# Optimization experiments

Measured on AMD Instinct MI355X. Metric: run time of the kernel, lower is better.

Reference implementation:

```python
import jax, jax.numpy as jnp
import numpy as np

CAPACITY_FACTOR = 1.25

def setup_inputs() -> dict:
    key = jax.random.key(0)
    ks = jax.random.split(key, 6)
    B, S, D, H, E = 4, 2048, 1024, 2048, 8
    x = jax.random.normal(ks[0], (B, S, D), dtype=jnp.float32)
    Wg = jax.random.normal(ks[1], (D, E), dtype=jnp.float32) / np.float32(np.sqrt(D))
    bg = jnp.zeros((E,), dtype=jnp.float32)
    W1 = jax.random.normal(ks[2], (E, H, D), dtype=jnp.float32) / np.float32(np.sqrt(H))
    W2 = jax.random.normal(ks[3], (E, D, H), dtype=jnp.float32) / np.float32(np.sqrt(D))
    W3 = jax.random.normal(ks[4], (E, D, H), dtype=jnp.float32) / np.float32(np.sqrt(D))
    return {"x": x, "Wg": Wg, "bg": bg, "W1": W1, "W2": W2, "W3": W3, "deterministic": 1}


def reference(x, Wg, bg, W1, W2, W3, deterministic):
    # deterministic=True path: no gate noise, no dropout (rate=0 anyway).
    b, s, d = x.shape
    E = W1.shape[0]
    xt = x.reshape(-1, d)                      # [N, d]
    N = xt.shape[0]
    cap = int(N / E * CAPACITY_FACTOR)

    logits = xt @ Wg + bg                      # [N, E]
    eid = jnp.argmax(logits, axis=1)           # [N] assigned expert (top-1)
    onehot = jax.nn.one_hot(eid, E, dtype=xt.dtype)
    # 0-based arrival position of each token within its expert's queue
    pos = (jnp.sum(jnp.cumsum(onehot, axis=0) * onehot, axis=1)).astype(jnp.int32) - 1
    valid = pos < cap                          # capacity mask (pos >= 0 always)
    slot = jnp.where(valid, pos, cap)          # overflow tokens -> dummy slot `cap`

    # Dispatch: scatter tokens into [E, cap+1, d]; slots unique among valid tokens
    buf = jnp.zeros((E, cap + 1, d), dtype=xt.dtype).at[eid, slot].set(xt)
    binp = buf[:, :cap]                        # [E, cap, d] (dummy slot dropped)

    # Grouped SwiGLU FFN per expert
    h = jax.nn.silu(jnp.einsum('ecd,edh->ech', binp, W2)) * jnp.einsum('ecd,edh->ech', binp, W3)
    bout = jnp.einsum('ech,ehd->ecd', h, W1)   # [E, cap, d]

    # Combine: gather each token's expert output; overflow tokens read zero row
    bout = jnp.concatenate([bout, jnp.zeros((E, 1, d), dtype=bout.dtype)], axis=1)
    eout = bout[eid, slot]                     # [N, d]

    weights = jax.nn.softmax(logits, axis=-1)
    gate_w = jnp.take_along_axis(weights, eid[:, None], axis=1)  # [N, 1]
    out = (gate_w * eout).reshape(b, s, d)
    return out
```

## Files before the change

### kernel.cpp

```cpp
#include <hip/hip_runtime.h>

#define N_TOK 8192
#define D_DIM 1024
#define H_DIM 2048
#define E_NUM 8
#define CAP   1280

typedef __attribute__((ext_vector_type(8))) short bf16x8;
typedef __attribute__((ext_vector_type(4))) float f32x4;

__device__ inline unsigned short f2bf(float f) {
  unsigned u = __float_as_uint(f);
  u += 0x7fffu + ((u >> 16) & 1u);
  return (unsigned short)(u >> 16);
}

#define VMCNT(n) asm volatile("s_waitcnt vmcnt(" #n ")" ::: "memory")
#define BARRIER() asm volatile("s_barrier" ::: "memory")

__global__ __launch_bounds__(256) void transpose_cvt_all(const float* __restrict__ W2,
                                                         const float* __restrict__ W3,
                                                         const float* __restrict__ W1,
                                                         unsigned short* __restrict__ w2t,
                                                         unsigned short* __restrict__ w3t,
                                                         unsigned short* __restrict__ w1t) {
  __shared__ float tile[64][33];
  const int id = blockIdx.x;
  const float* src;
  unsigned short* dst;
  int R, C, bx, by, b;
  if (id < 16384) {
    const int q = id & 8191;
    b = q >> 10;
    const int rem = q & 1023;
    bx = rem & 63;
    by = rem >> 6;
    R = D_DIM; C = H_DIM;
    src = (id < 8192 ? W2 : W3);
    dst = (id < 8192 ? w2t : w3t);
  } else {
    const int q = id - 16384;
    b = q >> 10;
    const int rem = q & 1023;
    bx = rem & 31;
    by = rem >> 5;
    R = H_DIM; C = D_DIM;
    src = W1; dst = w1t;
  }
  src += (size_t)b * R * C;
  dst += (size_t)b * R * C;
  const int c0 = bx * 32, r0 = by * 64;
  const int tx = threadIdx.x & 31, ty = threadIdx.x >> 5;
#pragma unroll
  for (int i = 0; i < 8; ++i)
    tile[ty + i * 8][tx] = src[(size_t)(r0 + ty + i * 8) * C + c0 + tx];
  __syncthreads();
  const int rp = threadIdx.x & 31;
  const int cb = threadIdx.x >> 5;
#pragma unroll
  for (int it = 0; it < 4; ++it) {
    const int c = cb + it * 8;
    unsigned short v[2] = {f2bf(tile[2 * rp][c]), f2bf(tile[2 * rp + 1][c])};
    *reinterpret_cast<unsigned*>(dst + (size_t)(c0 + c) * R + r0 + 2 * rp) =
        *reinterpret_cast<unsigned*>(v);
  }
}

__global__ __launch_bounds__(256) void gate_kernel(const float* __restrict__ x,
                                                   const float* __restrict__ Wg,
                                                   const float* __restrict__ bg,
                                                   int* __restrict__ eid,
                                                   float* __restrict__ gatew) {
  __shared__ float wg[E_NUM][D_DIM];
  const int tid = threadIdx.x;
  for (int i = tid; i < D_DIM * E_NUM; i += 256) {
    int d = i >> 3, e = i & 7;
    wg[e][d] = Wg[i];
  }
  __syncthreads();
  const int w = tid >> 6, l = tid & 63;
  const int t = blockIdx.x * 4 + w;
  const float* xr = x + (size_t)t * D_DIM;
  float acc[8] = {0, 0, 0, 0, 0, 0, 0, 0};
#pragma unroll
  for (int i = 0; i < D_DIM / 64; ++i) {
    float xv = xr[l + 64 * i];
#pragma unroll
    for (int e = 0; e < 8; ++e) acc[e] += xv * wg[e][l + 64 * i];
  }
#pragma unroll
  for (int off = 32; off >= 1; off >>= 1) {
#pragma unroll
    for (int e = 0; e < 8; ++e) acc[e] += __shfl_xor(acc[e], off);
  }
  if (l == 0) {
    float best = -1e30f;
    int bi = 0;
#pragma unroll
    for (int e = 0; e < 8; ++e) {
      acc[e] += bg[e];
      if (acc[e] > best) { best = acc[e]; bi = e; }
    }
    float s = 0.f;
#pragma unroll
    for (int e = 0; e < 8; ++e) s += __expf(acc[e] - best);
    eid[t] = bi;
    gatew[t] = 1.f / s;
  }
}

__global__ void scan_kernel(const int* __restrict__ eid, int* __restrict__ slot,
                            int* __restrict__ tok_of) {
  __shared__ int se[N_TOK];
  const int tid = threadIdx.x;
  for (int i = tid; i < N_TOK; i += 256) se[i] = eid[i];
  __syncthreads();
  if (tid >= 64) return;
  int counts[8] = {0, 0, 0, 0, 0, 0, 0, 0};
  const unsigned long long lower = (tid == 0) ? 0ull : ((1ull << tid) - 1ull);
  for (int base = 0; base < N_TOK; base += 64) {
    const int t = base + tid;
    const int e = se[t];
    int rank = 0;
#pragma unroll
    for (int ee = 0; ee < 8; ++ee) {
      unsigned long long m = __ballot(e == ee);
      if (e == ee) rank = counts[ee] + __popcll(m & lower);
      counts[ee] += __popcll(m);
    }
    slot[t] = rank < CAP ? rank : CAP;
    if (rank < CAP) tok_of[e * CAP + rank] = t;
  }
}

__global__ __launch_bounds__(256) void scatter_kernel(const float* __restrict__ x,
                                                      const int* __restrict__ tok_of,
                                                      unsigned short* __restrict__ binp) {
  const int row = blockIdx.x * 4 + (threadIdx.x >> 6);
  const int l = threadIdx.x & 63;
  const int t = tok_of[row];
  unsigned short* dst = binp + (size_t)row * D_DIM;
  if (t >= 0) {
    const float* src = x + (size_t)t * D_DIM;
#pragma unroll
    for (int i = 0; i < 4; ++i) {
      const int d = (i * 64 + l) * 4;
      float4 v = *reinterpret_cast<const float4*>(src + d);
      unsigned short r[4] = {f2bf(v.x), f2bf(v.y), f2bf(v.z), f2bf(v.w)};
      *reinterpret_cast<uint2*>(dst + d) = *reinterpret_cast<uint2*>(r);
    }
  } else {
    uint2 z = {0u, 0u};
#pragma unroll
    for (int i = 0; i < 4; ++i) {
      const int d = (i * 64 + l) * 4;
      *reinterpret_cast<uint2*>(dst + d) = z;
    }
  }
}

#define TILE64 (128 * 64)

__device__ inline void stage_tile(const unsigned short* __restrict__ g, int ldg, int k0,
                                  unsigned short* lds, int w, int l) {
  const int gcol = (l & 7) ^ (l >> 3);
  const unsigned short* gsrc = g + (size_t)(w * 32 + (l >> 3)) * ldg + k0 + gcol * 8;
#pragma unroll
  for (int it = 0; it < 4; ++it) {
    __builtin_amdgcn_global_load_lds(
        (const __attribute__((address_space(1))) unsigned int*)(gsrc + (size_t)(it * 8) * ldg),
        (__attribute__((address_space(3))) unsigned int*)(lds + (w * 32 + it * 8) * 64),
        16, 0, 0);
  }
}

__device__ inline bf16x8 lds_frag(const unsigned short* lds, int row, int c16) {
  return *reinterpret_cast<const bf16x8*>(lds + row * 64 + (c16 ^ (row & 7)) * 8);
}

__global__ __launch_bounds__(256, 2) void ffn1_kernel(const unsigned short* __restrict__ binp,
                                                      const unsigned short* __restrict__ w2t,
                                                      const unsigned short* __restrict__ w3t,
                                                      unsigned short* __restrict__ hbuf) {
  __shared__ unsigned short sA[2][TILE64], sB2[TILE64], sB3[TILE64];
  const int e = blockIdx.z, bx = blockIdx.x, by = blockIdx.y;
  const unsigned short* A  = binp + (size_t)e * CAP * D_DIM + (size_t)by * 128 * D_DIM;
  const unsigned short* B2 = w2t + (size_t)e * H_DIM * D_DIM + (size_t)bx * 128 * D_DIM;
  const unsigned short* B3 = w3t + (size_t)e * H_DIM * D_DIM + (size_t)bx * 128 * D_DIM;
  unsigned short* H = hbuf + (size_t)e * CAP * H_DIM;
  const int tid = threadIdx.x;
  const int l = tid & 63;
  const int w = tid >> 6, wr = w >> 1, wc = w & 1;
  f32x4 acc2[4][4] = {};
  f32x4 acc3[4][4] = {};

  stage_tile(A, D_DIM, 0, sA[0], w, l);

  const int NT = D_DIM / 64;
  int cur = 0;
  for (int kt = 0; kt < NT; ++kt) {
    stage_tile(B2, D_DIM, kt * 64, sB2, w, l);
    stage_tile(B3, D_DIM, kt * 64, sB3, w, l);
    if (kt + 1 < NT) {
      stage_tile(A, D_DIM, (kt + 1) * 64, sA[cur ^ 1], w, l);
      VMCNT(4);
    } else {
      VMCNT(0);
    }
    BARRIER();
#pragma unroll
    for (int kk = 0; kk < 2; ++kk) {
      const int c16 = kk * 4 + (l >> 4);
      bf16x8 af[4], b2f[4], b3f[4];
#pragma unroll
      for (int f = 0; f < 4; ++f) {
        af[f]  = lds_frag(sA[cur], wr * 64 + f * 16 + (l & 15), c16);
        b2f[f] = lds_frag(sB2, wc * 64 + f * 16 + (l & 15), c16);
        b3f[f] = lds_frag(sB3, wc * 64 + f * 16 + (l & 15), c16);
      }
#pragma unroll
      for (int fm = 0; fm < 4; ++fm)
#pragma unroll
        for (int fn = 0; fn < 4; ++fn) {
          acc2[fm][fn] = __builtin_amdgcn_mfma_f32_16x16x32_bf16(af[fm], b2f[fn], acc2[fm][fn], 0, 0, 0);
          acc3[fm][fn] = __builtin_amdgcn_mfma_f32_16x16x32_bf16(af[fm], b3f[fn], acc3[fm][fn], 0, 0, 0);
        }
    }
    BARRIER();
    cur ^= 1;
  }

  const int row0 = by * 128 + wr * 64;
  const int col0 = bx * 128 + wc * 64;
#pragma unroll
  for (int fm = 0; fm < 4; ++fm)
#pragma unroll
    for (int fn = 0; fn < 4; ++fn)
#pragma unroll
      for (int j = 0; j < 4; ++j) {
        const int row = row0 + fm * 16 + (l >> 4) * 4 + j;
        const int col = col0 + fn * 16 + (l & 15);
        const float v2 = acc2[fm][fn][j];
        const float v3 = acc3[fm][fn][j];
        const float hv = (v2 / (1.0f + __expf(-v2))) * v3;
        H[(size_t)row * H_DIM + col] = f2bf(hv);
      }
}

__global__ __launch_bounds__(256, 2) void ffn2_kernel(const unsigned short* __restrict__ hbuf,
                                                      const unsigned short* __restrict__ w1t,
                                                      const int* __restrict__ tok_of,
                                                      const float* __restrict__ gatew,
                                                      float* __restrict__ out) {
  __shared__ unsigned short sA[2][TILE64], sB[TILE64];
  const int e = blockIdx.z;
  const unsigned short* A = hbuf + (size_t)e * CAP * H_DIM + (size_t)blockIdx.y * 128 * H_DIM;
  const unsigned short* B = w1t + (size_t)e * D_DIM * H_DIM + (size_t)blockIdx.x * 128 * H_DIM;
  const int* tok = tok_of + e * CAP;
  const int tid = threadIdx.x;
  const int l = tid & 63;
  const int w = tid >> 6, wr = w >> 1, wc = w & 1;
  f32x4 acc[4][4] = {};

  stage_tile(A, H_DIM, 0, sA[0], w, l);

  const int NT = H_DIM / 64;
  int cur = 0;
  for (int kt = 0; kt < NT; ++kt) {
    stage_tile(B, H_DIM, kt * 64, sB, w, l);
    if (kt + 1 < NT) {
      stage_tile(A, H_DIM, (kt + 1) * 64, sA[cur ^ 1], w, l);
      VMCNT(4);
    } else {
      VMCNT(0);
    }
    BARRIER();
#pragma unroll
    for (int kk = 0; kk < 2; ++kk) {
      const int c16 = kk * 4 + (l >> 4);
      bf16x8 af[4], bfr[4];
#pragma unroll
      for (int f = 0; f < 4; ++f) {
        af[f]  = lds_frag(sA[cur], wr * 64 + f * 16 + (l & 15), c16);
        bfr[f] = lds_frag(sB, wc * 64 + f * 16 + (l & 15), c16);
      }
#pragma unroll
      for (int fm = 0; fm < 4; ++fm)
#pragma unroll
        for (int fn = 0; fn < 4; ++fn)
          acc[fm][fn] = __builtin_amdgcn_mfma_f32_16x16x32_bf16(af[fm], bfr[fn], acc[fm][fn], 0, 0, 0);
    }
    BARRIER();
    cur ^= 1;
  }

  const int row0 = blockIdx.y * 128 + wr * 64;
  const int col0 = blockIdx.x * 128 + wc * 64;
#pragma unroll
  for (int fm = 0; fm < 4; ++fm)
#pragma unroll
    for (int j = 0; j < 4; ++j) {
      const int row = row0 + fm * 16 + (l >> 4) * 4 + j;
      const int t = tok[row];
      if (t >= 0) {
        const float g = gatew[t];
#pragma unroll
        for (int fn = 0; fn < 4; ++fn) {
          const int col = col0 + fn * 16 + (l & 15);
          out[(size_t)t * D_DIM + col] = g * acc[fm][fn][j];
        }
      }
    }
}

__global__ __launch_bounds__(256) void zero_overflow(const int* __restrict__ slot,
                                                     float* __restrict__ out) {
  const int t = blockIdx.x * 4 + (threadIdx.x >> 6);
  if (slot[t] < CAP) return;
  const int l = threadIdx.x & 63;
  float4 z = {0.f, 0.f, 0.f, 0.f};
#pragma unroll
  for (int i = 0; i < 4; ++i)
    *reinterpret_cast<float4*>(out + (size_t)t * D_DIM + (i * 64 + l) * 4) = z;
}

extern "C" void kernel_launch(void* const* d_in, const int* in_sizes, int n_in,
                              void* d_out, int out_size, void* d_ws, size_t ws_size,
                              hipStream_t stream) {
  const float* x  = (const float*)d_in[0];
  const float* Wg = (const float*)d_in[1];
  const float* bg = (const float*)d_in[2];
  const float* W1 = (const float*)d_in[3];
  const float* W2 = (const float*)d_in[4];
  const float* W3 = (const float*)d_in[5];
  float* out = (float*)d_out;

  char* ws = (char*)d_ws;
  unsigned short* w2t = (unsigned short*)ws; ws += (size_t)E_NUM * H_DIM * D_DIM * 2;
  unsigned short* w3t = (unsigned short*)ws; ws += (size_t)E_NUM * H_DIM * D_DIM * 2;
  unsigned short* w1t = (unsigned short*)ws; ws += (size_t)E_NUM * D_DIM * H_DIM * 2;
  unsigned short* binp = (unsigned short*)ws; ws += (size_t)E_NUM * CAP * D_DIM * 2;
  unsigned short* hbuf = (unsigned short*)ws; ws += (size_t)E_NUM * CAP * H_DIM * 2;
  int* eid = (int*)ws;    ws += (size_t)N_TOK * 4;
  float* gw = (float*)ws; ws += (size_t)N_TOK * 4;
  int* slot = (int*)ws;   ws += (size_t)N_TOK * 4;
  int* tok_of = (int*)ws; ws += (size_t)E_NUM * CAP * 4;

  transpose_cvt_all<<<24576, 256, 0, stream>>>(W2, W3, W1, w2t, w3t, w1t);
  hipMemsetAsync(tok_of, 0xFF, (size_t)E_NUM * CAP * 4, stream);
  gate_kernel<<<N_TOK / 4, 256, 0, stream>>>(x, Wg, bg, eid, gw);
  scan_kernel<<<1, 256, 0, stream>>>(eid, slot, tok_of);
  scatter_kernel<<<E_NUM * CAP / 4, 256, 0, stream>>>(x, tok_of, binp);
  ffn1_kernel<<<dim3(H_DIM / 128, CAP / 128, E_NUM), 256, 0, stream>>>(binp, w2t, w3t, hbuf);
  ffn2_kernel<<<dim3(D_DIM / 128, CAP / 128, E_NUM), 256, 0, stream>>>(hbuf, w1t, tok_of, gw, out);
  zero_overflow<<<N_TOK / 4, 256, 0, stream>>>(slot, out);
}
```

Before: 264.9 us.

## Enlarge FFN1 tile, double-buffer B tiles, and remap blocks per XCD

FFN1 now runs 512 threads per block on a 256x128 output tile, so each W2/W3 tile staged into LDS is reused across twice as many token rows. Both FFN kernels now double-buffer the weight tiles as well as the activation tiles, and prefetch the next K-step while the current one computes. Both kernels also use a 1D grid with an id remap that keeps each expert's blocks on the same XCD, to improve L2 reuse. The trade-off is heavy register and LDS pressure: FFN1 holds two 4x4 accumulator sets, and its launch bound of (512, 2) may force register spills. Its roughly 128KB of LDS limits each CU to one block.

```diff
diff --git a/kernel.cpp b/kernel.cpp
--- a/kernel.cpp
+++ b/kernel.cpp
@@ -174,36 +174,57 @@
   }
 }
 
+__device__ inline void stage_tileB8(const unsigned short* __restrict__ g, int ldg, int k0,
+                                    unsigned short* lds, int w, int l) {
+  const int gcol = (l & 7) ^ (l >> 3);
+  const unsigned short* gsrc = g + (size_t)(w * 16 + (l >> 3)) * ldg + k0 + gcol * 8;
+#pragma unroll
+  for (int it = 0; it < 2; ++it) {
+    __builtin_amdgcn_global_load_lds(
+        (const __attribute__((address_space(1))) unsigned int*)(gsrc + (size_t)(it * 8) * ldg),
+        (__attribute__((address_space(3))) unsigned int*)(lds + (w * 16 + it * 8) * 64),
+        16, 0, 0);
+  }
+}
+
 __device__ inline bf16x8 lds_frag(const unsigned short* lds, int row, int c16) {
   return *reinterpret_cast<const bf16x8*>(lds + row * 64 + (c16 ^ (row & 7)) * 8);
 }
 
-__global__ __launch_bounds__(256, 2) void ffn1_kernel(const unsigned short* __restrict__ binp,
+__global__ __launch_bounds__(512, 2) void ffn1_kernel(const unsigned short* __restrict__ binp,
                                                       const unsigned short* __restrict__ w2t,
                                                       const unsigned short* __restrict__ w3t,
                                                       unsigned short* __restrict__ hbuf) {
-  __shared__ unsigned short sA[2][TILE64], sB2[TILE64], sB3[TILE64];
-  const int e = blockIdx.z, bx = blockIdx.x, by = blockIdx.y;
-  const unsigned short* A  = binp + (size_t)e * CAP * D_DIM + (size_t)by * 128 * D_DIM;
+  __shared__ unsigned short sA[2][256 * 64], sB2[2][TILE64], sB3[2][TILE64];
+  const int id = (blockIdx.x & 7) * 80 + (blockIdx.x >> 3);
+  const int e = id / 80;
+  const int rem = id - e * 80;
+  const int bx = rem / 5;
+  const int by = rem - bx * 5;
+  const unsigned short* A  = binp + (size_t)e * CAP * D_DIM + (size_t)by * 256 * D_DIM;
   const unsigned short* B2 = w2t + (size_t)e * H_DIM * D_DIM + (size_t)bx * 128 * D_DIM;
   const unsigned short* B3 = w3t + (size_t)e * H_DIM * D_DIM + (size_t)bx * 128 * D_DIM;
   unsigned short* H = hbuf + (size_t)e * CAP * H_DIM;
   const int tid = threadIdx.x;
   const int l = tid & 63;
-  const int w = tid >> 6, wr = w >> 1, wc = w & 1;
+  const int w = tid >> 6;
+  const int wr = w >> 1, wc = w & 1;
   f32x4 acc2[4][4] = {};
   f32x4 acc3[4][4] = {};
 
   stage_tile(A, D_DIM, 0, sA[0], w, l);
+  stage_tileB8(B2, D_DIM, 0, sB2[0], w, l);
+  stage_tileB8(B3, D_DIM, 0, sB3[0], w, l);
 
   const int NT = D_DIM / 64;
   int cur = 0;
   for (int kt = 0; kt < NT; ++kt) {
-    stage_tile(B2, D_DIM, kt * 64, sB2, w, l);
-    stage_tile(B3, D_DIM, kt * 64, sB3, w, l);
     if (kt + 1 < NT) {
-      stage_tile(A, D_DIM, (kt + 1) * 64, sA[cur ^ 1], w, l);
-      VMCNT(4);
+      const int nxt = cur ^ 1;
+      stage_tile(A, D_DIM, (kt + 1) * 64, sA[nxt], w, l);
+      stage_tileB8(B2, D_DIM, (kt + 1) * 64, sB2[nxt], w, l);
+      stage_tileB8(B3, D_DIM, (kt + 1) * 64, sB3[nxt], w, l);
+      VMCNT(8);
     } else {
       VMCNT(0);
     }
@@ -215,8 +236,8 @@
 #pragma unroll
       for (int f = 0; f < 4; ++f) {
         af[f]  = lds_frag(sA[cur], wr * 64 + f * 16 + (l & 15), c16);
-        b2f[f] = lds_frag(sB2, wc * 64 + f * 16 + (l & 15), c16);
-        b3f[f] = lds_frag(sB3, wc * 64 + f * 16 + (l & 15), c16);
+        b2f[f] = lds_frag(sB2[cur], wc * 64 + f * 16 + (l & 15), c16);
+        b3f[f] = lds_frag(sB3[cur], wc * 64 + f * 16 + (l & 15), c16);
       }
 #pragma unroll
       for (int fm = 0; fm < 4; ++fm)
@@ -230,7 +251,7 @@
     cur ^= 1;
   }
 
-  const int row0 = by * 128 + wr * 64;
+  const int row0 = by * 256 + wr * 64;
   const int col0 = bx * 128 + wc * 64;
 #pragma unroll
   for (int fm = 0; fm < 4; ++fm)
@@ -252,10 +273,14 @@
                                                       const int* __restrict__ tok_of,
                                                       const float* __restrict__ gatew,
                                                       float* __restrict__ out) {
-  __shared__ unsigned short sA[2][TILE64], sB[TILE64];
-  const int e = blockIdx.z;
-  const unsigned short* A = hbuf + (size_t)e * CAP * H_DIM + (size_t)blockIdx.y * 128 * H_DIM;
-  const unsigned short* B = w1t + (size_t)e * D_DIM * H_DIM + (size_t)blockIdx.x * 128 * H_DIM;
+  __shared__ unsigned short sA[2][TILE64], sB[2][TILE64];
+  const int id = (blockIdx.x & 7) * 80 + (blockIdx.x >> 3);
+  const int e = id / 80;
+  const int rem = id - e * 80;
+  const int bx = rem / 10;
+  const int by = rem - bx * 10;
+  const unsigned short* A = hbuf + (size_t)e * CAP * H_DIM + (size_t)by * 128 * H_DIM;
+  const unsigned short* B = w1t + (size_t)e * D_DIM * H_DIM + (size_t)bx * 128 * H_DIM;
   const int* tok = tok_of + e * CAP;
   const int tid = threadIdx.x;
   const int l = tid & 63;
@@ -263,14 +288,16 @@
   f32x4 acc[4][4] = {};
 
   stage_tile(A, H_DIM, 0, sA[0], w, l);
+  stage_tile(B, H_DIM, 0, sB[0], w, l);
 
   const int NT = H_DIM / 64;
   int cur = 0;
   for (int kt = 0; kt < NT; ++kt) {
-    stage_tile(B, H_DIM, kt * 64, sB, w, l);
     if (kt + 1 < NT) {
-      stage_tile(A, H_DIM, (kt + 1) * 64, sA[cur ^ 1], w, l);
-      VMCNT(4);
+      const int nxt = cur ^ 1;
+      stage_tile(A, H_DIM, (kt + 1) * 64, sA[nxt], w, l);
+      stage_tile(B, H_DIM, (kt + 1) * 64, sB[nxt], w, l);
+      VMCNT(8);
     } else {
       VMCNT(0);
     }
@@ -282,7 +309,7 @@
 #pragma unroll
       for (int f = 0; f < 4; ++f) {
         af[f]  = lds_frag(sA[cur], wr * 64 + f * 16 + (l & 15), c16);
-        bfr[f] = lds_frag(sB, wc * 64 + f * 16 + (l & 15), c16);
+        bfr[f] = lds_frag(sB[cur], wc * 64 + f * 16 + (l & 15), c16);
       }
 #pragma unroll
       for (int fm = 0; fm < 4; ++fm)
@@ -294,8 +321,8 @@
     cur ^= 1;
   }
 
-  const int row0 = blockIdx.y * 128 + wr * 64;
-  const int col0 = blockIdx.x * 128 + wc * 64;
+  const int row0 = by * 128 + wr * 64;
+  const int col0 = bx * 128 + wc * 64;
 #pragma unroll
   for (int fm = 0; fm < 4; ++fm)
 #pragma unroll
@@ -351,7 +378,7 @@
   gate_kernel<<<N_TOK / 4, 256, 0, stream>>>(x, Wg, bg, eid, gw);
   scan_kernel<<<1, 256, 0, stream>>>(eid, slot, tok_of);
   scatter_kernel<<<E_NUM * CAP / 4, 256, 0, stream>>>(x, tok_of, binp);
-  ffn1_kernel<<<dim3(H_DIM / 128, CAP / 128, E_NUM), 256, 0, stream>>>(binp, w2t, w3t, hbuf);
-  ffn2_kernel<<<dim3(D_DIM / 128, CAP / 128, E_NUM), 256, 0, stream>>>(hbuf, w1t, tok_of, gw, out);
+  ffn1_kernel<<<640, 512, 0, stream>>>(binp, w2t, w3t, hbuf);
+  ffn2_kernel<<<640, 256, 0, stream>>>(hbuf, w1t, tok_of, gw, out);
   zero_overflow<<<N_TOK / 4, 256, 0, stream>>>(slot, out);
 }
```

New measurement: 302.6 us. 14.2% more time.

## Prefetch weight tiles through registers and remap GEMM blocks per XCD

Applied to the files above, without the earlier changes.

Weight (B) tiles in both FFN GEMMs are now loaded into registers for the next K step while the current step computes, then written to swizzled LDS after a barrier. Previously they went straight into a single LDS buffer at the start of each iteration, so every step waited on them. Both grids are flattened to 1D, and a block-id remap groups each expert's tiles onto the same XCD (blockIdx & 7) to improve L2 reuse. The cost is more registers, an extra barrier plus an LDS write phase per iteration, and a full vmcnt(0) wait. A dead helper, load_breg, is added but never called.

```diff
diff --git a/kernel.cpp b/kernel.cpp
--- a/kernel.cpp
+++ b/kernel.cpp
@@ -7,6 +7,7 @@
 #define CAP   1280
 
 typedef __attribute__((ext_vector_type(8))) short bf16x8;
+typedef __attribute__((ext_vector_type(8))) unsigned short u16x8;
 typedef __attribute__((ext_vector_type(4))) float f32x4;
 
 __device__ inline unsigned short f2bf(float f) {
@@ -15,7 +16,8 @@
   return (unsigned short)(u >> 16);
 }
 
-#define VMCNT(n) asm volatile("s_waitcnt vmcnt(" #n ")" ::: "memory")
+#define VMCNT0() asm volatile("s_waitcnt vmcnt(0)" ::: "memory")
+#define LGKM0()  asm volatile("s_waitcnt lgkmcnt(0)" ::: "memory")
 #define BARRIER() asm volatile("s_barrier" ::: "memory")
 
 __global__ __launch_bounds__(256) void transpose_cvt_all(const float* __restrict__ W2,
@@ -174,6 +176,16 @@
   }
 }
 
+__device__ inline void load_breg(const unsigned short* __restrict__ g, int k0, int tid,
+                                 u16x8* r) {
+#pragma unroll
+  for (int it = 0; it < 4; ++it) {
+    const int row = it * 32 + (tid >> 3);
+    r[it] = *reinterpret_cast<const u16x8*>(g + (size_t)row * D_DIM * 0 + (size_t)row * 0 + 0
+                                            );
+  }
+}
+
 __device__ inline bf16x8 lds_frag(const unsigned short* lds, int row, int c16) {
   return *reinterpret_cast<const bf16x8*>(lds + row * 64 + (c16 ^ (row & 7)) * 8);
 }
@@ -183,7 +195,11 @@
                                                       const unsigned short* __restrict__ w3t,
                                                       unsigned short* __restrict__ hbuf) {
   __shared__ unsigned short sA[2][TILE64], sB2[TILE64], sB3[TILE64];
-  const int e = blockIdx.z, bx = blockIdx.x, by = blockIdx.y;
+  const int id = (blockIdx.x & 7) * 160 + (blockIdx.x >> 3);
+  const int e = id / 160;
+  const int rem = id - e * 160;
+  const int bx = rem / 10;
+  const int by = rem - bx * 10;
   const unsigned short* A  = binp + (size_t)e * CAP * D_DIM + (size_t)by * 128 * D_DIM;
   const unsigned short* B2 = w2t + (size_t)e * H_DIM * D_DIM + (size_t)bx * 128 * D_DIM;
   const unsigned short* B3 = w3t + (size_t)e * H_DIM * D_DIM + (size_t)bx * 128 * D_DIM;
@@ -194,20 +210,39 @@
   f32x4 acc2[4][4] = {};
   f32x4 acc3[4][4] = {};
 
+  const int brow = tid >> 3, bch = tid & 7;
+  u16x8 rb2[4], rb3[4];
+
   stage_tile(A, D_DIM, 0, sA[0], w, l);
+#pragma unroll
+  for (int it = 0; it < 4; ++it) {
+    const int row = it * 32 + brow;
+    rb2[it] = *reinterpret_cast<const u16x8*>(B2 + (size_t)row * D_DIM + bch * 8);
+    rb3[it] = *reinterpret_cast<const u16x8*>(B3 + (size_t)row * D_DIM + bch * 8);
+  }
+  VMCNT0();
+#pragma unroll
+  for (int it = 0; it < 4; ++it) {
+    const int row = it * 32 + brow;
+    const int ch = bch ^ (row & 7);
+    *reinterpret_cast<u16x8*>(&sB2[row * 64 + ch * 8]) = rb2[it];
+    *reinterpret_cast<u16x8*>(&sB3[row * 64 + ch * 8]) = rb3[it];
+  }
+  LGKM0();
+  BARRIER();
 
   const int NT = D_DIM / 64;
   int cur = 0;
   for (int kt = 0; kt < NT; ++kt) {
-    stage_tile(B2, D_DIM, kt * 64, sB2, w, l);
-    stage_tile(B3, D_DIM, kt * 64, sB3, w, l);
     if (kt + 1 < NT) {
       stage_tile(A, D_DIM, (kt + 1) * 64, sA[cur ^ 1], w, l);
-      VMCNT(4);
-    } else {
-      VMCNT(0);
-    }
-    BARRIER();
+#pragma unroll
+      for (int it = 0; it < 4; ++it) {
+        const int row = it * 32 + brow;
+        rb2[it] = *reinterpret_cast<const u16x8*>(B2 + (size_t)row * D_DIM + (kt + 1) * 64 + bch * 8);
+        rb3[it] = *reinterpret_cast<const u16x8*>(B3 + (size_t)row * D_DIM + (kt + 1) * 64 + bch * 8);
+      }
+    }
 #pragma unroll
     for (int kk = 0; kk < 2; ++kk) {
       const int c16 = kk * 4 + (l >> 4);
@@ -227,7 +262,19 @@
         }
     }
     BARRIER();
-    cur ^= 1;
+    if (kt + 1 < NT) {
+      VMCNT0();
+#pragma unroll
+      for (int it = 0; it < 4; ++it) {
+        const int row = it * 32 + brow;
+        const int ch = bch ^ (row & 7);
+        *reinterpret_cast<u16x8*>(&sB2[row * 64 + ch * 8]) = rb2[it];
+        *reinterpret_cast<u16x8*>(&sB3[row * 64 + ch * 8]) = rb3[it];
+      }
+      LGKM0();
+      BARRIER();
+      cur ^= 1;
+    }
   }
 
   const int row0 = by * 128 + wr * 64;
@@ -253,28 +300,49 @@
                                                       const float* __restrict__ gatew,
                                                       float* __restrict__ out) {
   __shared__ unsigned short sA[2][TILE64], sB[TILE64];
-  const int e = blockIdx.z;
-  const unsigned short* A = hbuf + (size_t)e * CAP * H_DIM + (size_t)blockIdx.y * 128 * H_DIM;
-  const unsigned short* B = w1t + (size_t)e * D_DIM * H_DIM + (size_t)blockIdx.x * 128 * H_DIM;
+  const int id = (blockIdx.x & 7) * 80 + (blockIdx.x >> 3);
+  const int e = id / 80;
+  const int rem = id - e * 80;
+  const int bx = rem / 10;
+  const int by = rem - bx * 10;
+  const unsigned short* A = hbuf + (size_t)e * CAP * H_DIM + (size_t)by * 128 * H_DIM;
+  const unsigned short* B = w1t + (size_t)e * D_DIM * H_DIM + (size_t)bx * 128 * H_DIM;
   const int* tok = tok_of + e * CAP;
   const int tid = threadIdx.x;
   const int l = tid & 63;
   const int w = tid >> 6, wr = w >> 1, wc = w & 1;
   f32x4 acc[4][4] = {};
 
+  const int brow = tid >> 3, bch = tid & 7;
+  u16x8 rb[4];
+
   stage_tile(A, H_DIM, 0, sA[0], w, l);
+#pragma unroll
+  for (int it = 0; it < 4; ++it) {
+    const int row = it * 32 + brow;
+    rb[it] = *reinterpret_cast<const u16x8*>(B + (size_t)row * H_DIM + bch * 8);
+  }
+  VMCNT0();
+#pragma unroll
+  for (int it = 0; it < 4; ++it) {
+    const int row = it * 32 + brow;
+    const int ch = bch ^ (row & 7);
+    *reinterpret_cast<u16x8*>(&sB[row * 64 + ch * 8]) = rb[it];
+  }
+  LGKM0();
+  BARRIER();
 
   const int NT = H_DIM / 64;
   int cur = 0;
   for (int kt = 0; kt < NT; ++kt) {
-    stage_tile(B, H_DIM, kt * 64, sB, w, l);
     if (kt + 1 < NT) {
       stage_tile(A, H_DIM, (kt + 1) * 64, sA[cur ^ 1], w, l);
-      VMCNT(4);
-    } else {
-      VMCNT(0);
-    }
-    BARRIER();
+#pragma unroll
+      for (int it = 0; it < 4; ++it) {
+        const int row = it * 32 + brow;
+        rb[it] = *reinterpret_cast<const u16x8*>(B + (size_t)row * H_DIM + (kt + 1) * 64 + bch * 8);
+      }
+    }
 #pragma unroll
     for (int kk = 0; kk < 2; ++kk) {
       const int c16 = kk * 4 + (l >> 4);
@@ -291,11 +359,22 @@
           acc[fm][fn] = __builtin_amdgcn_mfma_f32_16x16x32_bf16(af[fm], bfr[fn], acc[fm][fn], 0, 0, 0);
     }
     BARRIER();
-    cur ^= 1;
-  }
-
-  const int row0 = blockIdx.y * 128 + wr * 64;
-  const int col0 = blockIdx.x * 128 + wc * 64;
+    if (kt + 1 < NT) {
+      VMCNT0();
+#pragma unroll
+      for (int it = 0; it < 4; ++it) {
+        const int row = it * 32 + brow;
+        const int ch = bch ^ (row & 7);
+        *reinterpret_cast<u16x8*>(&sB[row * 64 + ch * 8]) = rb[it];
+      }
+      LGKM0();
+      BARRIER();
+      cur ^= 1;
+    }
+  }
+
+  const int row0 = by * 128 + wr * 64;
+  const int col0 = bx * 128 + wc * 64;
 #pragma unroll
   for (int fm = 0; fm < 4; ++fm)
 #pragma unroll
@@ -351,7 +430,7 @@
   gate_kernel<<<N_TOK / 4, 256, 0, stream>>>(x, Wg, bg, eid, gw);
   scan_kernel<<<1, 256, 0, stream>>>(eid, slot, tok_of);
   scatter_kernel<<<E_NUM * CAP / 4, 256, 0, stream>>>(x, tok_of, binp);
-  ffn1_kernel<<<dim3(H_DIM / 128, CAP / 128, E_NUM), 256, 0, stream>>>(binp, w2t, w3t, hbuf);
-  ffn2_kernel<<<dim3(D_DIM / 128, CAP / 128, E_NUM), 256, 0, stream>>>(hbuf, w1t, tok_of, gw, out);
+  ffn1_kernel<<<1280, 256, 0, stream>>>(binp, w2t, w3t, hbuf);
+  ffn2_kernel<<<640, 256, 0, stream>>>(hbuf, w1t, tok_of, gw, out);
   zero_overflow<<<N_TOK / 4, 256, 0, stream>>>(slot, out);
 }
```

New measurement: 274.8 us. 3.7% more time.

## Load A fragments directly to registers and double-buffer B tiles in FFN GEMMs

Applied to the files above, without the earlier changes.

Both FFN GEMM kernels now skip staging the activation (A) operand through LDS. Each wave loads its A fragments straight from global memory into registers, one K-tile ahead, with even/odd register buffers. The weight tiles are double-buffered in LDS so the next tile's load overlaps the current MFMAs, and s_setprio is raised around the MFMA bursts. A 1D grid with a remapped block index spreads experts across XCDs to improve L2 locality. In exchange, register pressure rises and the A loads are redundant across the two wc waves.

```diff
diff --git a/kernel.cpp b/kernel.cpp
--- a/kernel.cpp
+++ b/kernel.cpp
@@ -178,12 +178,61 @@
   return *reinterpret_cast<const bf16x8*>(lds + row * 64 + (c16 ^ (row & 7)) * 8);
 }
 
+__device__ __forceinline__ void ffn1_step(int kt, const unsigned short* B2,
+                                          const unsigned short* B3,
+                                          unsigned short (*sB2)[TILE64],
+                                          unsigned short (*sB3)[TILE64],
+                                          const unsigned short* aBase,
+                                          bf16x8* aC, bf16x8* aN,
+                                          f32x4 (&acc2)[4][4], f32x4 (&acc3)[4][4],
+                                          int w, int l, int wc) {
+  const int cur = kt & 1;
+  if (kt + 1 < 16) {
+    stage_tile(B2, D_DIM, (kt + 1) * 64, sB2[cur ^ 1], w, l);
+    stage_tile(B3, D_DIM, (kt + 1) * 64, sB3[cur ^ 1], w, l);
+#pragma unroll
+    for (int kk = 0; kk < 2; ++kk)
+#pragma unroll
+      for (int f = 0; f < 4; ++f)
+        aN[kk * 4 + f] = *reinterpret_cast<const bf16x8*>(
+            aBase + (size_t)f * 16 * D_DIM + (kt + 1) * 64 + kk * 32);
+    VMCNT(16);
+  } else {
+    VMCNT(0);
+  }
+  BARRIER();
+#pragma unroll
+  for (int kk = 0; kk < 2; ++kk) {
+    const int c16 = kk * 4 + (l >> 4);
+    bf16x8 b2f[4], b3f[4];
+#pragma unroll
+    for (int f = 0; f < 4; ++f) {
+      b2f[f] = lds_frag(sB2[cur], wc * 64 + f * 16 + (l & 15), c16);
+      b3f[f] = lds_frag(sB3[cur], wc * 64 + f * 16 + (l & 15), c16);
+    }
+    __builtin_amdgcn_s_setprio(1);
+#pragma unroll
+    for (int fm = 0; fm < 4; ++fm)
+#pragma unroll
+      for (int fn = 0; fn < 4; ++fn) {
+        acc2[fm][fn] = __builtin_amdgcn_mfma_f32_16x16x32_bf16(aC[kk * 4 + fm], b2f[fn], acc2[fm][fn], 0, 0, 0);
+        acc3[fm][fn] = __builtin_amdgcn_mfma_f32_16x16x32_bf16(aC[kk * 4 + fm], b3f[fn], acc3[fm][fn], 0, 0, 0);
+      }
+    __builtin_amdgcn_s_setprio(0);
+  }
+  BARRIER();
+}
+
 __global__ __launch_bounds__(256, 2) void ffn1_kernel(const unsigned short* __restrict__ binp,
                                                       const unsigned short* __restrict__ w2t,
                                                       const unsigned short* __restrict__ w3t,
                                                       unsigned short* __restrict__ hbuf) {
-  __shared__ unsigned short sA[2][TILE64], sB2[TILE64], sB3[TILE64];
-  const int e = blockIdx.z, bx = blockIdx.x, by = blockIdx.y;
+  __shared__ unsigned short sB2[2][TILE64], sB3[2][TILE64];
+  const int id = (blockIdx.x & 7) * 160 + (blockIdx.x >> 3);
+  const int e = id / 160;
+  const int rem = id - e * 160;
+  const int bx = rem / 10;
+  const int by = rem - bx * 10;
   const unsigned short* A  = binp + (size_t)e * CAP * D_DIM + (size_t)by * 128 * D_DIM;
   const unsigned short* B2 = w2t + (size_t)e * H_DIM * D_DIM + (size_t)bx * 128 * D_DIM;
   const unsigned short* B3 = w3t + (size_t)e * H_DIM * D_DIM + (size_t)bx * 128 * D_DIM;
@@ -191,43 +240,23 @@
   const int tid = threadIdx.x;
   const int l = tid & 63;
   const int w = tid >> 6, wr = w >> 1, wc = w & 1;
+  const unsigned short* aBase = A + (size_t)(wr * 64 + (l & 15)) * D_DIM + (l >> 4) * 8;
   f32x4 acc2[4][4] = {};
   f32x4 acc3[4][4] = {};
-
-  stage_tile(A, D_DIM, 0, sA[0], w, l);
-
-  const int NT = D_DIM / 64;
-  int cur = 0;
-  for (int kt = 0; kt < NT; ++kt) {
-    stage_tile(B2, D_DIM, kt * 64, sB2, w, l);
-    stage_tile(B3, D_DIM, kt * 64, sB3, w, l);
-    if (kt + 1 < NT) {
-      stage_tile(A, D_DIM, (kt + 1) * 64, sA[cur ^ 1], w, l);
-      VMCNT(4);
-    } else {
-      VMCNT(0);
-    }
-    BARRIER();
-#pragma unroll
-    for (int kk = 0; kk < 2; ++kk) {
-      const int c16 = kk * 4 + (l >> 4);
-      bf16x8 af[4], b2f[4], b3f[4];
-#pragma unroll
-      for (int f = 0; f < 4; ++f) {
-        af[f]  = lds_frag(sA[cur], wr * 64 + f * 16 + (l & 15), c16);
-        b2f[f] = lds_frag(sB2, wc * 64 + f * 16 + (l & 15), c16);
-        b3f[f] = lds_frag(sB3, wc * 64 + f * 16 + (l & 15), c16);
-      }
-#pragma unroll
-      for (int fm = 0; fm < 4; ++fm)
-#pragma unroll
-        for (int fn = 0; fn < 4; ++fn) {
-          acc2[fm][fn] = __builtin_amdgcn_mfma_f32_16x16x32_bf16(af[fm], b2f[fn], acc2[fm][fn], 0, 0, 0);
-          acc3[fm][fn] = __builtin_amdgcn_mfma_f32_16x16x32_bf16(af[fm], b3f[fn], acc3[fm][fn], 0, 0, 0);
-        }
-    }
-    BARRIER();
-    cur ^= 1;
+  bf16x8 aE[8], aO[8];
+
+  stage_tile(B2, D_DIM, 0, sB2[0], w, l);
+  stage_tile(B3, D_DIM, 0, sB3[0], w, l);
+#pragma unroll
+  for (int kk = 0; kk < 2; ++kk)
+#pragma unroll
+    for (int f = 0; f < 4; ++f)
+      aE[kk * 4 + f] = *reinterpret_cast<const bf16x8*>(
+          aBase + (size_t)f * 16 * D_DIM + kk * 32);
+
+  for (int kt2 = 0; kt2 < 16; kt2 += 2) {
+    ffn1_step(kt2,     B2, B3, sB2, sB3, aBase, aE, aO, acc2, acc3, w, l, wc);
+    ffn1_step(kt2 + 1, B2, B3, sB2, sB3, aBase, aO, aE, acc2, acc3, w, l, wc);
   }
 
   const int row0 = by * 128 + wr * 64;
@@ -247,55 +276,79 @@
       }
 }
 
+__device__ __forceinline__ void ffn2_step(int kt, const unsigned short* B,
+                                          unsigned short (*sB)[TILE64],
+                                          const unsigned short* aBase,
+                                          bf16x8* aC, bf16x8* aN,
+                                          f32x4 (&acc)[4][4], int w, int l, int wc) {
+  const int cur = kt & 1;
+  if (kt + 1 < 32) {
+    stage_tile(B, H_DIM, (kt + 1) * 64, sB[cur ^ 1], w, l);
+#pragma unroll
+    for (int kk = 0; kk < 2; ++kk)
+#pragma unroll
+      for (int f = 0; f < 4; ++f)
+        aN[kk * 4 + f] = *reinterpret_cast<const bf16x8*>(
+            aBase + (size_t)f * 16 * H_DIM + (kt + 1) * 64 + kk * 32);
+    VMCNT(12);
+  } else {
+    VMCNT(0);
+  }
+  BARRIER();
+#pragma unroll
+  for (int kk = 0; kk < 2; ++kk) {
+    const int c16 = kk * 4 + (l >> 4);
+    bf16x8 bfr[4];
+#pragma unroll
+    for (int f = 0; f < 4; ++f)
+      bfr[f] = lds_frag(sB[cur], wc * 64 + f * 16 + (l & 15), c16);
+    __builtin_amdgcn_s_setprio(1);
+#pragma unroll
+    for (int fm = 0; fm < 4; ++fm)
+#pragma unroll
+      for (int fn = 0; fn < 4; ++fn)
+        acc[fm][fn] = __builtin_amdgcn_mfma_f32_16x16x32_bf16(aC[kk * 4 + fm], bfr[fn], acc[fm][fn], 0, 0, 0);
+    __builtin_amdgcn_s_setprio(0);
+  }
+  BARRIER();
+}
+
 __global__ __launch_bounds__(256, 2) void ffn2_kernel(const unsigned short* __restrict__ hbuf,
                                                       const unsigned short* __restrict__ w1t,
                                                       const int* __restrict__ tok_of,
                                                       const float* __restrict__ gatew,
                                                       float* __restrict__ out) {
-  __shared__ unsigned short sA[2][TILE64], sB[TILE64];
-  const int e = blockIdx.z;
-  const unsigned short* A = hbuf + (size_t)e * CAP * H_DIM + (size_t)blockIdx.y * 128 * H_DIM;
-  const unsigned short* B = w1t + (size_t)e * D_DIM * H_DIM + (size_t)blockIdx.x * 128 * H_DIM;
+  __shared__ unsigned short sB[2][TILE64];
+  const int id = (blockIdx.x & 7) * 80 + (blockIdx.x >> 3);
+  const int e = id / 80;
+  const int rem = id - e * 80;
+  const int bx = rem / 10;
+  const int by = rem - bx * 10;
+  const unsigned short* A = hbuf + (size_t)e * CAP * H_DIM + (size_t)by * 128 * H_DIM;
+  const unsigned short* B = w1t + (size_t)e * D_DIM * H_DIM + (size_t)bx * 128 * H_DIM;
   const int* tok = tok_of + e * CAP;
   const int tid = threadIdx.x;
   const int l = tid & 63;
   const int w = tid >> 6, wr = w >> 1, wc = w & 1;
+  const unsigned short* aBase = A + (size_t)(wr * 64 + (l & 15)) * H_DIM + (l >> 4) * 8;
   f32x4 acc[4][4] = {};
-
-  stage_tile(A, H_DIM, 0, sA[0], w, l);
-
-  const int NT = H_DIM / 64;
-  int cur = 0;
-  for (int kt = 0; kt < NT; ++kt) {
-    stage_tile(B, H_DIM, kt * 64, sB, w, l);
-    if (kt + 1 < NT) {
-      stage_tile(A, H_DIM, (kt + 1) * 64, sA[cur ^ 1], w, l);
-      VMCNT(4);
-    } else {
-      VMCNT(0);
-    }
-    BARRIER();
-#pragma unroll
-    for (int kk = 0; kk < 2; ++kk) {
-      const int c16 = kk * 4 + (l >> 4);
-      bf16x8 af[4], bfr[4];
-#pragma unroll
-      for (int f = 0; f < 4; ++f) {
-        af[f]  = lds_frag(sA[cur], wr * 64 + f * 16 + (l & 15), c16);
-        bfr[f] = lds_frag(sB, wc * 64 + f * 16 + (l & 15), c16);
-      }
-#pragma unroll
-      for (int fm = 0; fm < 4; ++fm)
-#pragma unroll
-        for (int fn = 0; fn < 4; ++fn)
-          acc[fm][fn] = __builtin_amdgcn_mfma_f32_16x16x32_bf16(af[fm], bfr[fn], acc[fm][fn], 0, 0, 0);
-    }
-    BARRIER();
-    cur ^= 1;
-  }
-
-  const int row0 = blockIdx.y * 128 + wr * 64;
-  const int col0 = blockIdx.x * 128 + wc * 64;
+  bf16x8 aE[8], aO[8];
+
+  stage_tile(B, H_DIM, 0, sB[0], w, l);
+#pragma unroll
+  for (int kk = 0; kk < 2; ++kk)
+#pragma unroll
+    for (int f = 0; f < 4; ++f)
+      aE[kk * 4 + f] = *reinterpret_cast<const bf16x8*>(
+          aBase + (size_t)f * 16 * H_DIM + kk * 32);
+
+  for (int kt2 = 0; kt2 < 32; kt2 += 2) {
+    ffn2_step(kt2,     B, sB, aBase, aE, aO, acc, w, l, wc);
+    ffn2_step(kt2 + 1, B, sB, aBase, aO, aE, acc, w, l, wc);
+  }
+
+  const int row0 = by * 128 + wr * 64;
+  const int col0 = bx * 128 + wc * 64;
 #pragma unroll
   for (int fm = 0; fm < 4; ++fm)
 #pragma unroll
@@ -351,7 +404,7 @@
   gate_kernel<<<N_TOK / 4, 256, 0, stream>>>(x, Wg, bg, eid, gw);
   scan_kernel<<<1, 256, 0, stream>>>(eid, slot, tok_of);
   scatter_kernel<<<E_NUM * CAP / 4, 256, 0, stream>>>(x, tok_of, binp);
-  ffn1_kernel<<<dim3(H_DIM / 128, CAP / 128, E_NUM), 256, 0, stream>>>(binp, w2t, w3t, hbuf);
-  ffn2_kernel<<<dim3(D_DIM / 128, CAP / 128, E_NUM), 256, 0, stream>>>(hbuf, w1t, tok_of, gw, out);
+  ffn1_kernel<<<1280, 256, 0, stream>>>(binp, w2t, w3t, hbuf);
+  ffn2_kernel<<<640, 256, 0, stream>>>(hbuf, w1t, tok_of, gw, out);
   zero_overflow<<<N_TOK / 4, 256, 0, stream>>>(slot, out);
 }
```

New measurement: 578.4 us. 2.18x slower.
